# Kernel optimization log

Measured on AMD Instinct MI355X. Metric: run time of the kernel, lower is better.

## Reference

```python
import jax, jax.numpy as jnp
import numpy as np

POS_SIZE = 63
LATENT_SIZE = 256
NUM_CLUSTERS = 64
N = 524288


def setup_inputs() -> dict:
    key = jax.random.key(0)
    k1, k2, k3, k4 = jax.random.split(key, 4)
    X = jax.random.normal(k1, (N, POS_SIZE + LATENT_SIZE), dtype=jnp.float32)
    cluster_ids = jax.random.randint(k2, (N,), 0, NUM_CLUSTERS, dtype=jnp.int32)
    # nn.Linear weights have shape [out_features, in_features]
    W_pos = jax.random.normal(k3, (3 * NUM_CLUSTERS, POS_SIZE), dtype=jnp.float32) * 0.1
    W_feat = jax.random.normal(k4, (3 * NUM_CLUSTERS, LATENT_SIZE), dtype=jnp.float32) * 0.1
    return {"X": X, "cluster_ids": cluster_ids, "W_pos": W_pos, "W_feat": W_feat}


def reference(X, cluster_ids, W_pos, W_feat):
    # Dense projections: [N, 3*num_clusters]
    rgb_clusters = (
        jnp.einsum("np,cp->nc", X[:, :POS_SIZE], W_pos)
        + jnp.einsum("nl,cl->nc", X[:, POS_SIZE:], W_feat)
    )
    # Per-row gather of the 3 columns belonging to this row's cluster.
    cols = 3 * cluster_ids[:, None] + jnp.arange(3, dtype=cluster_ids.dtype)[None, :]  # [N, 3]
    rgb = jnp.take_along_axis(rgb_clusters, cols, axis=1)  # [N, 3]
    return rgb
```

## Files before the change

### kernel.cpp

```cpp
#include <hip/hip_runtime.h>


constexpr int POS = 63, LAT = 256, DIM = 319, NCH = 192;
constexpr int ROWS = 32;
constexpr int PW_DW = NCH * 160;
constexpr size_t PW_BYTES = (size_t)PW_DW * 4;
constexpr int TILE_DW = ROWS * DIM;
constexpr int TILE_F4 = TILE_DW / 4;
constexpr int TPB = 16;

typedef __attribute__((ext_vector_type(8))) short short8;
typedef __attribute__((ext_vector_type(4))) float f32x4;

__device__ __forceinline__ unsigned f2bf(float f) {
    unsigned u = __float_as_uint(f);
    return (u + 0x7fffu + ((u >> 16) & 1u)) >> 16;
}

__global__ __launch_bounds__(256) void pack_weights(
    const float* __restrict__ Wp, const float* __restrict__ Wf,
    unsigned* __restrict__ pw)
{
    const int idx = blockIdx.x * 256 + threadIdx.x;
    if (idx >= PW_DW) return;
    const int ch = idx / 160, d = idx - ch * 160;
    auto wat = [&](int k) -> float {
        if (k < POS) return Wp[ch * POS + k];
        if (k < DIM) return Wf[ch * LAT + (k - POS)];
        return 0.f;
    };
    pw[idx] = f2bf(wat(2 * d)) | (f2bf(wat(2 * d + 1)) << 16);
}

__global__ __launch_bounds__(256, 2) void lad_mfma2(
    const float4* __restrict__ X4, const int* __restrict__ cid,
    const unsigned* __restrict__ pw, float* __restrict__ out,
    int ntiles)
{
    __shared__ float xb[2][TILE_DW];

    const int thr = threadIdx.x;
    const int l   = thr & 63;
    const int wid = thr >> 6;
    const int n0  = wid * 48;
    const int cl  = l & 15;
    const int q   = l >> 4;

    short8 Bf[3][10];
#pragma unroll
    for (int nt = 0; nt < 3; ++nt)
#pragma unroll
        for (int kk = 0; kk < 10; ++kk)
            Bf[nt][kk] = *reinterpret_cast<const short8*>(
                pw + (size_t)(n0 + nt * 16 + cl) * 160 + kk * 16 + q * 4);

    const int t0 = blockIdx.x * TPB;
    const int tend = min(t0 + TPB, ntiles);
    if (t0 >= tend) return;

    auto stage = [&](int tile, int p) {
        const float4* src = X4 + (size_t)tile * TILE_F4;
#pragma unroll
        for (int j = 0; j < 10; ++j) {
            const int slot = j * 256 + thr;
            if (slot < TILE_F4)
                __builtin_amdgcn_global_load_lds(
                    (const __attribute__((address_space(1))) unsigned int*)(src + slot),
                    (__attribute__((address_space(3))) unsigned int*)&xb[p][slot * 4],
                    16, 0, 0);
        }
    };

    stage(t0, 0);
    __syncthreads();

    int p = 0;
    for (int t = t0; t < tend; ++t) {
        if (t + 1 < tend) stage(t + 1, p ^ 1);

        int c3v[2][4];
#pragma unroll
        for (int mt = 0; mt < 2; ++mt)
#pragma unroll
            for (int j = 0; j < 4; ++j)
                c3v[mt][j] = 3 * cid[(size_t)t * ROWS + mt * 16 + q * 4 + j];

        f32x4 acc[2][3];
#pragma unroll
        for (int mt = 0; mt < 2; ++mt)
#pragma unroll
            for (int nt = 0; nt < 3; ++nt)
                acc[mt][nt] = (f32x4)0.0f;

#pragma unroll
        for (int kk = 0; kk < 10; ++kk) {
            short8 Af[2];
#pragma unroll
            for (int mt = 0; mt < 2; ++mt) {
                const float* fp = &xb[p][(mt * 16 + cl) * DIM + kk * 32 + q * 8];
                union { unsigned u[4]; short8 s; } cv;
#pragma unroll
                for (int h = 0; h < 4; ++h) {
                    asm("v_cvt_pk_bf16_f32 %0, %1, %2"
                        : "=v"(cv.u[h]) : "v"(fp[2 * h]), "v"(fp[2 * h + 1]));
                }
                Af[mt] = cv.s;
            }
#pragma unroll
            for (int mt = 0; mt < 2; ++mt)
#pragma unroll
                for (int nt = 0; nt < 3; ++nt)
                    acc[mt][nt] = __builtin_amdgcn_mfma_f32_16x16x32_bf16(
                        Af[mt], Bf[nt][kk], acc[mt][nt], 0, 0, 0);
        }

#pragma unroll
        for (int mt = 0; mt < 2; ++mt)
#pragma unroll
            for (int j = 0; j < 4; ++j) {
                const int grow = t * ROWS + mt * 16 + q * 4 + j;
                const int c3 = c3v[mt][j];
#pragma unroll
                for (int nt = 0; nt < 3; ++nt) {
                    const int col = n0 + nt * 16 + cl;
                    const unsigned d = (unsigned)(col - c3);
                    if (d < 3u)
                        out[(size_t)grow * 3 + d] = acc[mt][nt][j];
                }
            }

        __syncthreads();
        p ^= 1;
    }
}

template <int CTRL>
__device__ __forceinline__ float dpp_add_step(float x) {
    int s = __builtin_amdgcn_update_dpp(0, __float_as_int(x), CTRL,
                                        0xF, 0xF, true);
    return x + __int_as_float(s);
}
__device__ __forceinline__ float wave_reduce_sum(float x) {
    x = dpp_add_step<0x111>(x);
    x = dpp_add_step<0x112>(x);
    x = dpp_add_step<0x114>(x);
    x = dpp_add_step<0x118>(x);
    x = dpp_add_step<0x142>(x);
    x = dpp_add_step<0x143>(x);
    return x;
}

__global__ __launch_bounds__(256) void lad_fallback(
    const float* __restrict__ X, const int* __restrict__ cid,
    const float* __restrict__ Wp, const float* __restrict__ Wf,
    float* __restrict__ out, int n)
{
    const int lane = threadIdx.x & 63;
    const int wave = (int)((blockIdx.x * blockDim.x + threadIdx.x) >> 6);
    if (wave >= n) return;
    const size_t row = (size_t)wave;
    const float* xrow = X + row * (size_t)DIM;
    const float* xf   = xrow + POS;
    const int c3 = cid[row] * 3;
    const float* wp0 = Wp + (size_t)c3 * POS;
    const float* wf0 = Wf + (size_t)c3 * LAT;
    float a0 = 0.f, a1 = 0.f, a2 = 0.f;
#pragma unroll
    for (int i = 0; i < 4; ++i) {
        const int k = lane + 64 * i;
        const float x = xf[k];
        a0 = fmaf(x, wf0[k], a0);
        a1 = fmaf(x, wf0[k + LAT], a1);
        a2 = fmaf(x, wf0[k + 2 * LAT], a2);
    }
    if (lane < POS) {
        const float x = xrow[lane];
        a0 = fmaf(x, wp0[lane], a0);
        a1 = fmaf(x, wp0[lane + POS], a1);
        a2 = fmaf(x, wp0[lane + 2 * POS], a2);
    }
    a0 = wave_reduce_sum(a0);
    a1 = wave_reduce_sum(a1);
    a2 = wave_reduce_sum(a2);
    if (lane == 63) {
        float* o = out + row * 3;
        o[0] = a0; o[1] = a1; o[2] = a2;
    }
}

extern "C" void kernel_launch(void* const* d_in, const int* in_sizes, int n_in,
                              void* d_out, int out_size, void* d_ws, size_t ws_size,
                              hipStream_t stream) {
    const float* X   = (const float*)d_in[0];
    const int*   cid = (const int*)d_in[1];
    const float* Wp  = (const float*)d_in[2];
    const float* Wf  = (const float*)d_in[3];
    float* out = (float*)d_out;
    const int n = in_sizes[1];

    if (ws_size >= PW_BYTES && n > 0 && (n % ROWS) == 0) {
        unsigned* pw = (unsigned*)d_ws;
        pack_weights<<<(PW_DW + 255) / 256, 256, 0, stream>>>(Wp, Wf, pw);
        const int ntiles = n / ROWS;
        const int grid = (ntiles + TPB - 1) / TPB;
        lad_mfma2<<<grid, 256, 0, stream>>>((const float4*)X, cid, pw, out,
                                            ntiles);
    } else {
        const int blocks = (n + 3) / 4;
        lad_fallback<<<blocks, 256, 0, stream>>>(X, cid, Wp, Wf, out, n);
    }
}
```

Measured before the change: 153.9 us.

## Halve row tile to raise occupancy and use a fixed persistent grid

Shrinks the per-tile row count from 32 to 16, which halves the LDS double buffer and the accumulator registers so three blocks per CU can be resident instead of two. The launch switches to a fixed grid of 768 blocks, each looping over a computed number of tiles, in place of a fixed tiles-per-block count. The goal is more latency hiding for the streaming X loads. In exchange each tile does half the MFMA work per sync and per staging round, so there is more barrier and loop overhead per row.

```diff
diff --git a/kernel.cpp b/kernel.cpp
--- a/kernel.cpp
+++ b/kernel.cpp
@@ -2,12 +2,12 @@
 
 
 constexpr int POS = 63, LAT = 256, DIM = 319, NCH = 192;
-constexpr int ROWS = 32;
+constexpr int ROWS = 16;
 constexpr int PW_DW = NCH * 160;
 constexpr size_t PW_BYTES = (size_t)PW_DW * 4;
 constexpr int TILE_DW = ROWS * DIM;
 constexpr int TILE_F4 = TILE_DW / 4;
-constexpr int TPB = 16;
+constexpr int GRID = 768;
 
 typedef __attribute__((ext_vector_type(8))) short short8;
 typedef __attribute__((ext_vector_type(4))) float f32x4;
@@ -32,10 +32,10 @@
     pw[idx] = f2bf(wat(2 * d)) | (f2bf(wat(2 * d + 1)) << 16);
 }
 
-__global__ __launch_bounds__(256, 2) void lad_mfma2(
+__global__ __launch_bounds__(256, 3) void lad_mfma3(
     const float4* __restrict__ X4, const int* __restrict__ cid,
     const unsigned* __restrict__ pw, float* __restrict__ out,
-    int ntiles)
+    int ntiles, int tpb)
 {
     __shared__ float xb[2][TILE_DW];
 
@@ -54,14 +54,14 @@
             Bf[nt][kk] = *reinterpret_cast<const short8*>(
                 pw + (size_t)(n0 + nt * 16 + cl) * 160 + kk * 16 + q * 4);
 
-    const int t0 = blockIdx.x * TPB;
-    const int tend = min(t0 + TPB, ntiles);
+    const int t0 = blockIdx.x * tpb;
+    const int tend = min(t0 + tpb, ntiles);
     if (t0 >= tend) return;
 
     auto stage = [&](int tile, int p) {
         const float4* src = X4 + (size_t)tile * TILE_F4;
 #pragma unroll
-        for (int j = 0; j < 10; ++j) {
+        for (int j = 0; j < 5; ++j) {
             const int slot = j * 256 + thr;
             if (slot < TILE_F4)
                 __builtin_amdgcn_global_load_lds(
@@ -78,56 +78,43 @@
     for (int t = t0; t < tend; ++t) {
         if (t + 1 < tend) stage(t + 1, p ^ 1);
 
-        int c3v[2][4];
+        int c3v[4];
 #pragma unroll
-        for (int mt = 0; mt < 2; ++mt)
+        for (int j = 0; j < 4; ++j)
+            c3v[j] = 3 * cid[(size_t)t * ROWS + q * 4 + j];
+
+        f32x4 acc[3];
 #pragma unroll
-            for (int j = 0; j < 4; ++j)
-                c3v[mt][j] = 3 * cid[(size_t)t * ROWS + mt * 16 + q * 4 + j];
-
-        f32x4 acc[2][3];
-#pragma unroll
-        for (int mt = 0; mt < 2; ++mt)
-#pragma unroll
-            for (int nt = 0; nt < 3; ++nt)
-                acc[mt][nt] = (f32x4)0.0f;
+        for (int nt = 0; nt < 3; ++nt)
+            acc[nt] = (f32x4)0.0f;
 
 #pragma unroll
         for (int kk = 0; kk < 10; ++kk) {
-            short8 Af[2];
+            const float* fp = &xb[p][cl * DIM + kk * 32 + q * 8];
+            union { unsigned u[4]; short8 s; } cv;
 #pragma unroll
-            for (int mt = 0; mt < 2; ++mt) {
-                const float* fp = &xb[p][(mt * 16 + cl) * DIM + kk * 32 + q * 8];
-                union { unsigned u[4]; short8 s; } cv;
-#pragma unroll
-                for (int h = 0; h < 4; ++h) {
-                    asm("v_cvt_pk_bf16_f32 %0, %1, %2"
-                        : "=v"(cv.u[h]) : "v"(fp[2 * h]), "v"(fp[2 * h + 1]));
-                }
-                Af[mt] = cv.s;
+            for (int h = 0; h < 4; ++h) {
+                asm("v_cvt_pk_bf16_f32 %0, %1, %2"
+                    : "=v"(cv.u[h]) : "v"(fp[2 * h]), "v"(fp[2 * h + 1]));
             }
 #pragma unroll
-            for (int mt = 0; mt < 2; ++mt)
-#pragma unroll
-                for (int nt = 0; nt < 3; ++nt)
-                    acc[mt][nt] = __builtin_amdgcn_mfma_f32_16x16x32_bf16(
-                        Af[mt], Bf[nt][kk], acc[mt][nt], 0, 0, 0);
+            for (int nt = 0; nt < 3; ++nt)
+                acc[nt] = __builtin_amdgcn_mfma_f32_16x16x32_bf16(
+                    cv.s, Bf[nt][kk], acc[nt], 0, 0, 0);
         }
 
 #pragma unroll
-        for (int mt = 0; mt < 2; ++mt)
+        for (int j = 0; j < 4; ++j) {
+            const int grow = t * ROWS + q * 4 + j;
+            const int c3 = c3v[j];
 #pragma unroll
-            for (int j = 0; j < 4; ++j) {
-                const int grow = t * ROWS + mt * 16 + q * 4 + j;
-                const int c3 = c3v[mt][j];
-#pragma unroll
-                for (int nt = 0; nt < 3; ++nt) {
-                    const int col = n0 + nt * 16 + cl;
-                    const unsigned d = (unsigned)(col - c3);
-                    if (d < 3u)
-                        out[(size_t)grow * 3 + d] = acc[mt][nt][j];
-                }
+            for (int nt = 0; nt < 3; ++nt) {
+                const int col = n0 + nt * 16 + cl;
+                const unsigned d = (unsigned)(col - c3);
+                if (d < 3u)
+                    out[(size_t)grow * 3 + d] = acc[nt][j];
             }
+        }
 
         __syncthreads();
         p ^= 1;
@@ -202,9 +189,9 @@
         unsigned* pw = (unsigned*)d_ws;
         pack_weights<<<(PW_DW + 255) / 256, 256, 0, stream>>>(Wp, Wf, pw);
         const int ntiles = n / ROWS;
-        const int grid = (ntiles + TPB - 1) / TPB;
-        lad_mfma2<<<grid, 256, 0, stream>>>((const float4*)X, cid, pw, out,
-                                            ntiles);
+        const int tpb = (ntiles + GRID - 1) / GRID;
+        lad_mfma3<<<GRID, 256, 0, stream>>>((const float4*)X, cid, pw, out,
+                                            ntiles, tpb);
     } else {
         const int blocks = (n + 3) / 4;
         lad_fallback<<<blocks, 256, 0, stream>>>(X, cid, Wp, Wf, out, n);
```

After: 146.8 us (median of 2 runs). 4.6% less time.
